# Optimization experiments

Measured on AMD Instinct MI355X. Metric: run time of the kernel, lower is better.

The kernel has to match this reference:

```python
import jax, jax.numpy as jnp
import numpy as np

N_NODES, N_EDGES, N_GRAPHS = 100000, 1600000, 1000
DIN, DMID, DGLOB, DOUT = 128, 128, 64, 2


def setup_inputs() -> dict:
    key = jax.random.key(0)
    ks = jax.random.split(key, 12)
    x = jax.random.normal(ks[0], (N_NODES, DIN), dtype=jnp.float32)
    edge_index = jax.random.randint(ks[1], (2, N_EDGES), 0, N_NODES, dtype=jnp.int64 if jax.config.jax_enable_x64 else jnp.int32)
    u = jax.random.normal(ks[2], (N_GRAPHS, DGLOB), dtype=jnp.float32)
    batch = jnp.sort(jax.random.randint(ks[3], (N_NODES,), 0, N_GRAPHS))
    s = 1.0 / np.sqrt(DMID)
    W1 = jax.random.normal(ks[4], (DIN, DMID), dtype=jnp.float32) * s
    b1 = jnp.zeros((DMID,), dtype=jnp.float32)
    W2 = jax.random.normal(ks[5], (DMID, DMID), dtype=jnp.float32) * s
    b2 = jnp.zeros((DMID,), dtype=jnp.float32)
    Wh1 = jax.random.normal(ks[6], (DMID + DGLOB, DMID), dtype=jnp.float32) * s
    bh1 = jnp.zeros((DMID,), dtype=jnp.float32)
    Wh2 = jax.random.normal(ks[7], (DMID, DOUT), dtype=jnp.float32) * s
    bh2 = jnp.zeros((DOUT,), dtype=jnp.float32)
    return {"x": x, "edge_index": edge_index, "u": u, "batch": batch,
            "batch_size": N_GRAPHS, "W1": W1, "b1": b1, "W2": W2, "b2": b2,
            "Wh1": Wh1, "bh1": bh1, "Wh2": Wh2, "bh2": bh2}


def _gcn_conv(x, W, b, row, col, norm, n):
    # PyG GCNConv: linear transform then symmetric-normalized scatter-add
    h = x @ W                                    # [N, dmid]
    msg = norm[:, None] * h[row]                 # gather along source nodes
    out = jax.ops.segment_sum(msg, col, num_segments=n)  # scatter to dst
    return out + b


def reference(x, edge_index, u, batch, batch_size, W1, b1, W2, b2, Wh1, bh1, Wh2, bh2):
    n = x.shape[0]
    # add self-loops (GCNConv default, edge_weight=None -> all-ones weights)
    loop = jnp.arange(n, dtype=edge_index.dtype)
    row = jnp.concatenate([edge_index[0], loop])
    col = jnp.concatenate([edge_index[1], loop])
    deg = jax.ops.segment_sum(jnp.ones_like(col, dtype=x.dtype), col, num_segments=n)
    dinv = jnp.where(deg > 0, jax.lax.rsqrt(jnp.maximum(deg, 1e-12)), 0.0)
    norm = dinv[row] * dinv[col]                 # D^-1/2 A D^-1/2, shared by both layers

    h = jax.nn.relu(_gcn_conv(x, W1, b1, row, col, norm, n))
    h = jax.nn.relu(_gcn_conv(h, W2, b2, row, col, norm, n))

    # mean pool per graph
    sums = jax.ops.segment_sum(h, batch, num_segments=batch_size)
    cnt = jax.ops.segment_sum(jnp.ones((n,), dtype=h.dtype), batch, num_segments=batch_size)
    graph_emb = sums / jnp.maximum(cnt, 1.0)[:, None]

    hcat = jnp.concatenate([graph_emb, u], axis=-1)
    # head MLP (dropout in eval mode = identity)
    out = jax.nn.relu(hcat @ Wh1 + bh1) @ Wh2 + bh2
    return out
```

## Files before the change

kernel.cpp:

```cpp
#include <hip/hip_runtime.h>
#include <hip/hip_bf16.h>

#define NN 100000
#define NE 1600000
#define NG 1000
#define NBK 196
#define BSH 9
#define SLOT 10240

typedef short short8 __attribute__((ext_vector_type(8)));
typedef float f32x4 __attribute__((ext_vector_type(4)));
typedef float f32x2 __attribute__((ext_vector_type(2)));

static inline int cdiv(int a, int b) { return (a + b - 1) / b; }

__device__ __forceinline__ unsigned short f2b(float f) {
    unsigned int u = __float_as_uint(f);
    u += 0x7fff + ((u >> 16) & 1);
    return (unsigned short)(u >> 16);
}
__device__ __forceinline__ unsigned int pack2(float lo, float hi) {
    return (unsigned int)f2b(lo) | ((unsigned int)f2b(hi) << 16);
}

template <int W>
__device__ __forceinline__ f32x2 f8_2f(unsigned int v) {
    return __builtin_amdgcn_cvt_pk_f32_fp8((int)v, W);
}
__device__ __forceinline__ unsigned int f2f8_lo(float a, float b, unsigned int old) {
    return (unsigned int)__builtin_amdgcn_cvt_pk_fp8_f32(a, b, (int)old, false);
}
__device__ __forceinline__ unsigned int f2f8_hi(float a, float b, unsigned int old) {
    return (unsigned int)__builtin_amdgcn_cvt_pk_fp8_f32(a, b, (int)old, true);
}
__device__ __forceinline__ unsigned char f2f8s(float a) {
    return (unsigned char)(__builtin_amdgcn_cvt_pk_fp8_f32(a, a, 0, false) & 0xFF);
}

__global__ __launch_bounds__(256) void k_prep(const float* __restrict__ W1,
                                              const float* __restrict__ W2,
                                              const float* __restrict__ b1,
                                              const float* __restrict__ b2,
                                              unsigned short* __restrict__ Wt1,
                                              unsigned char* __restrict__ Wt2p,
                                              float* __restrict__ b1p,
                                              float* __restrict__ b2p,
                                              int* __restrict__ gcur) {
    int b = blockIdx.x, t = threadIdx.x;
    if (b < 128) {
        if (t < 128) {
            Wt1[b * 128 + t] = f2b(W1[t * 128 + b]);
        } else {
            int q = t - 128;
            int c = (q & 7) * 16 + (q >> 3);
            Wt2p[b * 128 + q] = f2f8s(W2[c * 128 + b]);
        }
    } else {
        if (t < NBK) gcur[t] = t * SLOT;
        if (t < 128) {
            int c = (t & 7) * 16 + (t >> 3);
            b1p[t] = b1[c];
            b2p[t] = b2[c];
        }
    }
}

__global__ __launch_bounds__(256) void k_bin2(const int* __restrict__ row,
                                              const int* __restrict__ col,
                                              int* __restrict__ gcur,
                                              unsigned int* __restrict__ tmp) {
    __shared__ unsigned int ent[4000];
    __shared__ unsigned int srt[4000];
    __shared__ unsigned char bkt[4000];
    __shared__ unsigned char bky[4000];
    __shared__ int cnt[NBK];
    __shared__ int gbase[NBK];
    __shared__ int lbase[NBK];
    __shared__ int sh[256];
    int t = threadIdx.x;
    if (t < NBK) cnt[t] = 0;
    __syncthreads();
    const int q0 = blockIdx.x * 1000;
    const int4* col4 = (const int4*)col;
    const int4* row4 = (const int4*)row;
#pragma unroll
    for (int it = 0; it < 4; it++) {
        int idx = it * 256 + t;
        if (idx < 1000) {
            int4 c = col4[q0 + idx];
            int4 r = row4[q0 + idx];
            int d, b;
            d = c.x; b = d >> BSH; atomicAdd(&cnt[b], 1);
            ent[idx * 4 + 0] = ((unsigned int)(d & 511) << 17) | (unsigned int)r.x;
            bkt[idx * 4 + 0] = (unsigned char)b;
            d = c.y; b = d >> BSH; atomicAdd(&cnt[b], 1);
            ent[idx * 4 + 1] = ((unsigned int)(d & 511) << 17) | (unsigned int)r.y;
            bkt[idx * 4 + 1] = (unsigned char)b;
            d = c.z; b = d >> BSH; atomicAdd(&cnt[b], 1);
            ent[idx * 4 + 2] = ((unsigned int)(d & 511) << 17) | (unsigned int)r.z;
            bkt[idx * 4 + 2] = (unsigned char)b;
            d = c.w; b = d >> BSH; atomicAdd(&cnt[b], 1);
            ent[idx * 4 + 3] = ((unsigned int)(d & 511) << 17) | (unsigned int)r.w;
            bkt[idx * 4 + 3] = (unsigned char)b;
        }
    }
    __syncthreads();
    int v = (t < NBK) ? cnt[t] : 0;
    sh[t] = v;
    __syncthreads();
    for (int d = 1; d < 256; d <<= 1) {
        int u = (t >= d) ? sh[t - d] : 0;
        __syncthreads();
        sh[t] += u;
        __syncthreads();
    }
    if (t < NBK) {
        lbase[t] = sh[t] - v;
        gbase[t] = atomicAdd(&gcur[t], v);
        cnt[t] = sh[t] - v;
    }
    __syncthreads();
#pragma unroll
    for (int it = 0; it < 16; it++) {
        int i = it * 256 + t;
        if (i < 4000) {
            int b = bkt[i];
            int p = atomicAdd(&cnt[b], 1);
            srt[p] = ent[i];
            bky[p] = (unsigned char)b;
        }
    }
    __syncthreads();
#pragma unroll
    for (int it = 0; it < 16; it++) {
        int i = it * 256 + t;
        if (i < 4000) {
            int b = bky[i];
            tmp[gbase[b] + (i - lbase[b])] = srt[i];
        }
    }
}

__global__ __launch_bounds__(1024) void k_bucket(const unsigned int* __restrict__ tmp,
                                                 const int* __restrict__ gcur,
                                                 int* __restrict__ off,
                                                 int* __restrict__ degw,
                                                 float* __restrict__ dinv,
                                                 int* __restrict__ csr_src) {
    __shared__ int cnt[512];
    __shared__ int loff[512];
    __shared__ int sh[256];
    int b = blockIdx.x, t = threadIdx.x;
    int j0 = b << BSH;
    int nd = min(512, NN - j0);
    int rb = b * SLOT;
    int m = gcur[b] - rb;
    if (t < 512) cnt[t] = 0;
    __syncthreads();
    for (int i = t; i < m; i += 1024)
        atomicAdd(&cnt[tmp[rb + i] >> 17], 1);
    __syncthreads();
    int r0 = 0, r1 = 0, p0 = 0, ts = 0;
    if (t < 256) {
        r0 = cnt[2 * t]; r1 = cnt[2 * t + 1];
        p0 = (r0 + 3) & ~3;
        int p1 = (r1 + 3) & ~3;
        ts = p0 + p1;
        sh[t] = ts;
    }
    __syncthreads();
    for (int d = 1; d < 256; d <<= 1) {
        int u = (t >= d && t < 256) ? sh[t - d] : 0;
        __syncthreads();
        if (t < 256) sh[t] += u;
        __syncthreads();
    }
    if (t < 256) {
        int ex = sh[t] - ts;
        loff[2 * t] = ex;
        loff[2 * t + 1] = ex + p0;
    }
    __syncthreads();
    for (int j = t; j < nd; j += 1024) {
        int o = rb + loff[j];
        int dg = cnt[j];
        off[j0 + j] = o;
        degw[j0 + j] = dg;
        dinv[j0 + j] = rsqrtf((float)(dg + 1));
        cnt[j] = o;
    }
    __syncthreads();
    for (int i = t; i < m; i += 1024) {
        unsigned int e = tmp[rb + i];
        int d = e >> 17;
        int s = (int)(e & 0x1FFFFu);
        int p = atomicAdd(&cnt[d], 1);
        csr_src[p] = s;
    }
}

__global__ __launch_bounds__(256) void k_gemm1(const float* __restrict__ X,
                                               const unsigned short* __restrict__ Wt,
                                               const float* __restrict__ dinv,
                                               unsigned char* __restrict__ Hs8) {
    __shared__ __align__(16) unsigned short Ws[128 * 128];
    int t = threadIdx.x;
#pragma unroll
    for (int i = 0; i < 8; i++) {
        int id = t + i * 256;
        int n = id >> 4, c = id & 15;
        *(short8*)((char*)Ws + n * 256 + ((c ^ (n & 15)) << 4)) =
            *(const short8*)(Wt + n * 128 + c * 8);
    }
    __syncthreads();

    int lane = t & 63, wid = t >> 6;
    int n16 = lane & 15, quad = lane >> 4;
    int row_base = blockIdx.x * 128 + wid * 32;

    short8 a[2][4];
#pragma unroll
    for (int rt = 0; rt < 2; rt++) {
        int r = row_base + rt * 16 + n16;
        if (r > NN - 1) r = NN - 1;
        const float* ap = X + (size_t)r * 128 + quad * 8;
#pragma unroll
        for (int ks = 0; ks < 4; ks++) {
            float4 v0 = *(const float4*)(ap + ks * 32);
            float4 v1 = *(const float4*)(ap + ks * 32 + 4);
            uint4 up;
            up.x = pack2(v0.x, v0.y); up.y = pack2(v0.z, v0.w);
            up.z = pack2(v1.x, v1.y); up.w = pack2(v1.z, v1.w);
            a[rt][ks] = *(short8*)&up;
        }
    }

    f32x4 acc[2][8];
#pragma unroll
    for (int rt = 0; rt < 2; rt++)
#pragma unroll
        for (int ct = 0; ct < 8; ct++)
            acc[rt][ct] = (f32x4){0.f, 0.f, 0.f, 0.f};

#pragma unroll
    for (int ks = 0; ks < 4; ks++) {
#pragma unroll
        for (int ct = 0; ct < 8; ct++) {
            short8 b = *(const short8*)((const char*)Ws +
                        (ct * 16 + n16) * 256 + ((((ks << 2) + quad) ^ n16) << 4));
            acc[0][ct] = __builtin_amdgcn_mfma_f32_16x16x32_bf16(a[0][ks], b, acc[0][ct], 0, 0, 0);
            acc[1][ct] = __builtin_amdgcn_mfma_f32_16x16x32_bf16(a[1][ks], b, acc[1][ct], 0, 0, 0);
        }
    }

#pragma unroll
    for (int rt = 0; rt < 2; rt++) {
#pragma unroll
        for (int reg = 0; reg < 4; reg++) {
            int row = row_base + rt * 16 + quad * 4 + reg;
            if (row < NN) {
                float di = dinv[row];
                unsigned int u0 = 0, u1 = 0;
                u0 = f2f8_lo(acc[rt][0][reg] * di, acc[rt][1][reg] * di, u0);
                u0 = f2f8_hi(acc[rt][2][reg] * di, acc[rt][3][reg] * di, u0);
                u1 = f2f8_lo(acc[rt][4][reg] * di, acc[rt][5][reg] * di, u1);
                u1 = f2f8_hi(acc[rt][6][reg] * di, acc[rt][7][reg] * di, u1);
                uint2 o; o.x = u0; o.y = u1;
                ((uint2*)(Hs8 + (size_t)row * 128))[n16] = o;
            }
        }
    }
}

__global__ __launch_bounds__(256) void k_gemm2(const unsigned char* __restrict__ A8,
                                               const unsigned char* __restrict__ Wt2p,
                                               const float* __restrict__ dinv,
                                               unsigned char* __restrict__ Hs8) {
    __shared__ __align__(16) unsigned char Ws[128 * 128];
    int t = threadIdx.x;
#pragma unroll
    for (int i = 0; i < 8; i++) {
        int id = t + i * 256;
        int n = id >> 4, c = id & 15;
        *(uint2*)(Ws + n * 128 + ((c ^ (n & 15)) << 3)) =
            *(const uint2*)(Wt2p + n * 128 + c * 8);
    }
    __syncthreads();

    int lane = t & 63, wid = t >> 6;
    int n16 = lane & 15, quad = lane >> 4;
    int row_base = blockIdx.x * 128 + wid * 32;

    uint2 a[2][4];
#pragma unroll
    for (int rt = 0; rt < 2; rt++) {
        int r = row_base + rt * 16 + n16;
        if (r > NN - 1) r = NN - 1;
        const unsigned char* ap = A8 + (size_t)r * 128 + quad * 8;
#pragma unroll
        for (int ks = 0; ks < 4; ks++)
            a[rt][ks] = *(const uint2*)(ap + ks * 32);
    }

    f32x4 acc[2][8];
#pragma unroll
    for (int rt = 0; rt < 2; rt++)
#pragma unroll
        for (int ct = 0; ct < 8; ct++)
            acc[rt][ct] = (f32x4){0.f, 0.f, 0.f, 0.f};

#pragma unroll
    for (int ks = 0; ks < 4; ks++) {
        long a0 = __builtin_bit_cast(long, a[0][ks]);
        long a1 = __builtin_bit_cast(long, a[1][ks]);
#pragma unroll
        for (int ct = 0; ct < 8; ct++) {
            uint2 bv = *(const uint2*)(Ws + (ct * 16 + n16) * 128 +
                                       ((((ks << 2) + quad) ^ n16) << 3));
            long bb = __builtin_bit_cast(long, bv);
            acc[0][ct] = __builtin_amdgcn_mfma_f32_16x16x32_fp8_fp8(a0, bb, acc[0][ct], 0, 0, 0);
            acc[1][ct] = __builtin_amdgcn_mfma_f32_16x16x32_fp8_fp8(a1, bb, acc[1][ct], 0, 0, 0);
        }
    }

#pragma unroll
    for (int rt = 0; rt < 2; rt++) {
#pragma unroll
        for (int reg = 0; reg < 4; reg++) {
            int row = row_base + rt * 16 + quad * 4 + reg;
            if (row < NN) {
                float di = dinv[row];
                unsigned int u0 = 0, u1 = 0;
                u0 = f2f8_lo(acc[rt][0][reg] * di, acc[rt][1][reg] * di, u0);
                u0 = f2f8_hi(acc[rt][2][reg] * di, acc[rt][3][reg] * di, u0);
                u1 = f2f8_lo(acc[rt][4][reg] * di, acc[rt][5][reg] * di, u1);
                u1 = f2f8_hi(acc[rt][6][reg] * di, acc[rt][7][reg] * di, u1);
                uint2 o; o.x = u0; o.y = u1;
                ((uint2*)(Hs8 + (size_t)row * 128))[n16] = o;
            }
        }
    }
}

__global__ __launch_bounds__(256) void k_agg(const unsigned char* __restrict__ Hb,
                                             const int* __restrict__ off,
                                             const int* __restrict__ degw,
                                             const int* __restrict__ csr_src,
                                             const float* __restrict__ dinv,
                                             const float* __restrict__ biasp,
                                             unsigned char* __restrict__ outp) {
    int node = blockIdx.x * 4 + (threadIdx.x >> 6);
    int lane = threadIdx.x & 63;
    int sub = lane >> 4, li = lane & 15;
    unsigned loff = (unsigned)li * 8u;
    f32x2 A0 = {0.f, 0.f}, A1 = {0.f, 0.f}, A2 = {0.f, 0.f}, A3 = {0.f, 0.f};
#define LDH(idx) (*(const uint2*)(Hb + (unsigned)(idx) * 128u + loff))
#define ACC8(V) { \
        A0 += f8_2f<0>((V).x); A1 += f8_2f<1>((V).x); \
        A2 += f8_2f<0>((V).y); A3 += f8_2f<1>((V).y); }
    int deg = degw[node];
    int base = off[node];
    int slot = sub * 4;
    int4 iA = *(const int4*)(csr_src + base + slot);
    int4 iB;
    bool hasB = deg > 16;
    if (hasB) iB = *(const int4*)(csr_src + base + 16 + slot);
    uint2 v = {0, 0};
    if (sub == 0) v = LDH(node);
    uint2 w0 = {0,0}, w1 = {0,0}, w2 = {0,0}, w3 = {0,0};
    uint2 w4 = {0,0}, w5 = {0,0}, w6 = {0,0}, w7 = {0,0};
    if (slot + 0 < deg) w0 = LDH(iA.x);
    if (slot + 1 < deg) w1 = LDH(iA.y);
    if (slot + 2 < deg) w2 = LDH(iA.z);
    if (slot + 3 < deg) w3 = LDH(iA.w);
    if (hasB) {
        if (slot + 16 < deg) w4 = LDH(iB.x);
        if (slot + 17 < deg) w5 = LDH(iB.y);
        if (slot + 18 < deg) w6 = LDH(iB.z);
        if (slot + 19 < deg) w7 = LDH(iB.w);
    }
    ACC8(v)
    ACC8(w0) ACC8(w1) ACC8(w2) ACC8(w3)
    if (hasB) { ACC8(w4) ACC8(w5) ACC8(w6) ACC8(w7) }
    if (deg > 32) {
        int e = base + 32, e1 = base + deg;
        for (; e + 16 <= e1; e += 16) {
            int4 sv = *(const int4*)(csr_src + e + sub * 4);
            uint2 x0 = LDH(sv.x);
            uint2 x1 = LDH(sv.y);
            uint2 x2 = LDH(sv.z);
            uint2 x3 = LDH(sv.w);
            ACC8(x0) ACC8(x1) ACC8(x2) ACC8(x3)
        }
        for (; e + 8 <= e1; e += 8) {
            int2 sv = *(const int2*)(csr_src + e + sub * 2);
            uint2 xA = LDH(sv.x);
            uint2 xB = LDH(sv.y);
            ACC8(xA) ACC8(xB)
        }
        for (; e < e1; e += 4) {
            int ee = e + sub;
            if (ee < e1) {
                uint2 w = LDH(csr_src[ee]);
                ACC8(w)
            }
        }
    }
#undef ACC8
#undef LDH
#pragma unroll
    for (int d = 16; d <= 32; d <<= 1) {
        A0[0] += __shfl_xor(A0[0], d); A0[1] += __shfl_xor(A0[1], d);
        A1[0] += __shfl_xor(A1[0], d); A1[1] += __shfl_xor(A1[1], d);
        A2[0] += __shfl_xor(A2[0], d); A2[1] += __shfl_xor(A2[1], d);
        A3[0] += __shfl_xor(A3[0], d); A3[1] += __shfl_xor(A3[1], d);
    }
    if (sub == 0) {
        float di = dinv[node];
        const float4* b4 = (const float4*)biasp;
        float4 bA = b4[li * 2], bB = b4[li * 2 + 1];
        float r0 = fmaxf(fmaf(di, A0[0], bA.x), 0.f);
        float r1 = fmaxf(fmaf(di, A0[1], bA.y), 0.f);
        float r2 = fmaxf(fmaf(di, A1[0], bA.z), 0.f);
        float r3 = fmaxf(fmaf(di, A1[1], bA.w), 0.f);
        float r4 = fmaxf(fmaf(di, A2[0], bB.x), 0.f);
        float r5 = fmaxf(fmaf(di, A2[1], bB.y), 0.f);
        float r6 = fmaxf(fmaf(di, A3[0], bB.z), 0.f);
        float r7 = fmaxf(fmaf(di, A3[1], bB.w), 0.f);
        unsigned int u0 = 0, u1 = 0;
        u0 = f2f8_lo(r0, r1, u0); u0 = f2f8_hi(r2, r3, u0);
        u1 = f2f8_lo(r4, r5, u1); u1 = f2f8_hi(r6, r7, u1);
        uint2 o; o.x = u0; o.y = u1;
        *(uint2*)(outp + (unsigned)node * 128u + loff) = o;
    }
}

__global__ __launch_bounds__(256) void k_poolhead(const unsigned char* __restrict__ A,
                                                  const int* __restrict__ batch,
                                                  const float* __restrict__ u,
                                                  const float* __restrict__ Wh1,
                                                  const float* __restrict__ bh1,
                                                  const float* __restrict__ Wh2,
                                                  const float* __restrict__ bh2,
                                                  float* __restrict__ out) {
    int g = blockIdx.x, t = threadIdx.x;
    int lo = 0, hi = NN;
    while (lo < hi) { int m = (lo + hi) >> 1; if (batch[m] < g) lo = m + 1; else hi = m; }
    int start = lo;
    hi = NN;
    while (lo < hi) { int m = (lo + hi) >> 1; if (batch[m] < g + 1) lo = m + 1; else hi = m; }
    int end = lo;

    int li = t & 7;
    int ri = t >> 3;
    float acc[16];
#pragma unroll
    for (int j = 0; j < 16; j++) acc[j] = 0.f;
    f32x2 p;
    for (int i = start + ri; i < end; i += 32) {
        uint4 v = ((const uint4*)A)[(size_t)i * 8 + li];
#define UP(VV, base) p = f8_2f<0>(VV); acc[base] += p.x; acc[base+1] += p.y; \
                     p = f8_2f<1>(VV); acc[base+2] += p.x; acc[base+3] += p.y;
        UP(v.x, 0) UP(v.y, 4) UP(v.z, 8) UP(v.w, 12)
#undef UP
    }
#pragma unroll
    for (int j = 0; j < 16; j++) {
        acc[j] += __shfl_xor(acc[j], 8);
        acc[j] += __shfl_xor(acc[j], 16);
        acc[j] += __shfl_xor(acc[j], 32);
    }
    __shared__ float part[4][128];
    __shared__ float hc[192];
    __shared__ float tt[128];
    int w = t >> 6;
    if ((t & 63) < 8) {
#pragma unroll
        for (int j = 0; j < 16; j++) part[w][li * 16 + j] = acc[j];
    }
    __syncthreads();
    float cntf = (float)max(end - start, 1);
    if (t < 128) {
        int q = (t & 15) * 8 + (t >> 4);
        hc[t] = (part[0][q] + part[1][q] + part[2][q] + part[3][q]) / cntf;
    } else if (t < 192) {
        hc[t] = u[g * 64 + (t - 128)];
    }
    __syncthreads();
    if (t < 128) {
        float a2 = bh1[t];
        for (int k = 0; k < 192; k++) a2 = fmaf(hc[k], Wh1[k * 128 + t], a2);
        tt[t] = fmaxf(a2, 0.f);
    }
    __syncthreads();
    if (t < 2) {
        float o = bh2[t];
        for (int c2 = 0; c2 < 128; c2++) o = fmaf(tt[c2], Wh2[c2 * 2 + t], o);
        out[g * 2 + t] = o;
    }
}

extern "C" void kernel_launch(void* const* d_in, const int* in_sizes, int n_in,
                              void* d_out, int out_size, void* d_ws, size_t ws_size,
                              hipStream_t stream) {
    const float* x   = (const float*)d_in[0];
    const int*   ei  = (const int*)d_in[1];
    const int*   row = ei;
    const int*   col = ei + NE;
    const float* u   = (const float*)d_in[2];
    const int*   batch = (const int*)d_in[3];
    const float* W1  = (const float*)d_in[5];
    const float* b1  = (const float*)d_in[6];
    const float* W2  = (const float*)d_in[7];
    const float* b2  = (const float*)d_in[8];
    const float* Wh1 = (const float*)d_in[9];
    const float* bh1 = (const float*)d_in[10];
    const float* Wh2 = (const float*)d_in[11];
    const float* bh2 = (const float*)d_in[12];
    float* out = (float*)d_out;

    char* ws = (char*)d_ws;
    size_t o = 0;
    auto alloc = [&](size_t bytes) -> void* {
        void* p = ws + o;
        o += (bytes + 511) & ~(size_t)511;
        return p;
    };
    unsigned char*  Hs8 = (unsigned char*)alloc((size_t)NN * 128);
    unsigned char*  A1b = (unsigned char*)alloc((size_t)NN * 128);
    unsigned char*  A2b = (unsigned char*)alloc((size_t)NN * 128);
    unsigned short* Wt1 = (unsigned short*)alloc((size_t)128 * 128 * 2);
    unsigned char*  Wt2p= (unsigned char*)alloc((size_t)128 * 128);
    float* b1p    = (float*)alloc((size_t)128 * 4);
    float* b2p    = (float*)alloc((size_t)128 * 4);
    float* dinv   = (float*)alloc((size_t)NN * 4);
    int*   off    = (int*)alloc((size_t)NN * 4);
    int*   degw   = (int*)alloc((size_t)NN * 4);
    int*   csr_src= (int*)alloc((size_t)NBK * SLOT * 4 + 256);
    unsigned int* tmp = (unsigned int*)alloc((size_t)NBK * SLOT * 4);
    int*   gcur   = (int*)alloc((size_t)256 * 4);

    k_prep<<<129, 256, 0, stream>>>(W1, W2, b1, b2, Wt1, Wt2p, b1p, b2p, gcur);
    k_bin2<<<400, 256, 0, stream>>>(row, col, gcur, tmp);
    k_bucket<<<NBK, 1024, 0, stream>>>(tmp, gcur, off, degw, dinv, csr_src);

    k_gemm1<<<cdiv(NN, 128), 256, 0, stream>>>(x, Wt1, dinv, Hs8);
    k_agg<<<NN / 4, 256, 0, stream>>>(Hs8, off, degw, csr_src, dinv, b1p, A1b);
    k_gemm2<<<cdiv(NN, 128), 256, 0, stream>>>(A1b, Wt2p, dinv, Hs8);
    k_agg<<<NN / 4, 256, 0, stream>>>(Hs8, off, degw, csr_src, dinv, b2p, A2b);

    k_poolhead<<<NG, 256, 0, stream>>>(A2b, batch, u, Wh1, bh1, Wh2, bh2, out);
}
```

Before: 267.6 us.

## Use 16-lane group per node in aggregation; precompute graph start offsets

The aggregation kernel now assigns one 16-lane group to each node (16 nodes per block) instead of a full 64-lane wavefront that split edges four ways and reduced them with cross-lane shuffles. Each group walks its node's edges sequentially in chunks of four, which removes the shuffle reduction and the idle lanes during the epilogue. The trade-off is less memory-level parallelism per node and longer serial loops for high-degree nodes. Separately, k_prep gains extra blocks that compute per-graph start offsets from the sorted batch array, so the pooling kernel no longer runs two binary searches per graph.

Measured after the change: 259.3 us. 3.1% less time.

```diff
diff --git a/kernel.cpp b/kernel.cpp
--- a/kernel.cpp
+++ b/kernel.cpp
@@ -45,7 +45,9 @@
                                               unsigned char* __restrict__ Wt2p,
                                               float* __restrict__ b1p,
                                               float* __restrict__ b2p,
-                                              int* __restrict__ gcur) {
+                                              int* __restrict__ gcur,
+                                              const int* __restrict__ batch,
+                                              int* __restrict__ gstart) {
     int b = blockIdx.x, t = threadIdx.x;
     if (b < 128) {
         if (t < 128) {
@@ -55,12 +57,19 @@
             int c = (q & 7) * 16 + (q >> 3);
             Wt2p[b * 128 + q] = f2f8s(W2[c * 128 + b]);
         }
-    } else {
+    } else if (b == 128) {
         if (t < NBK) gcur[t] = t * SLOT;
         if (t < 128) {
             int c = (t & 7) * 16 + (t >> 3);
             b1p[t] = b1[c];
             b2p[t] = b2[c];
+        }
+    } else {
+        int n = (b - 129) * 256 + t;
+        if (n <= NN) {
+            int cur = (n == NN) ? NG : batch[n];
+            int prev = (n == 0) ? -1 : batch[n - 1];
+            for (int g = prev + 1; g <= cur; g++) gstart[g] = n;
         }
     }
 }
@@ -349,9 +358,8 @@
                                              const float* __restrict__ dinv,
                                              const float* __restrict__ biasp,
                                              unsigned char* __restrict__ outp) {
-    int node = blockIdx.x * 4 + (threadIdx.x >> 6);
-    int lane = threadIdx.x & 63;
-    int sub = lane >> 4, li = lane & 15;
+    int node = blockIdx.x * 16 + (threadIdx.x >> 4);
+    int li = threadIdx.x & 15;
     unsigned loff = (unsigned)li * 8u;
     f32x2 A0 = {0.f, 0.f}, A1 = {0.f, 0.f}, A2 = {0.f, 0.f}, A3 = {0.f, 0.f};
 #define LDH(idx) (*(const uint2*)(Hb + (unsigned)(idx) * 128u + loff))
@@ -360,83 +368,39 @@
         A2 += f8_2f<0>((V).y); A3 += f8_2f<1>((V).y); }
     int deg = degw[node];
     int base = off[node];
-    int slot = sub * 4;
-    int4 iA = *(const int4*)(csr_src + base + slot);
-    int4 iB;
-    bool hasB = deg > 16;
-    if (hasB) iB = *(const int4*)(csr_src + base + 16 + slot);
-    uint2 v = {0, 0};
-    if (sub == 0) v = LDH(node);
-    uint2 w0 = {0,0}, w1 = {0,0}, w2 = {0,0}, w3 = {0,0};
-    uint2 w4 = {0,0}, w5 = {0,0}, w6 = {0,0}, w7 = {0,0};
-    if (slot + 0 < deg) w0 = LDH(iA.x);
-    if (slot + 1 < deg) w1 = LDH(iA.y);
-    if (slot + 2 < deg) w2 = LDH(iA.z);
-    if (slot + 3 < deg) w3 = LDH(iA.w);
-    if (hasB) {
-        if (slot + 16 < deg) w4 = LDH(iB.x);
-        if (slot + 17 < deg) w5 = LDH(iB.y);
-        if (slot + 18 < deg) w6 = LDH(iB.z);
-        if (slot + 19 < deg) w7 = LDH(iB.w);
-    }
+    uint2 v = LDH(node);
     ACC8(v)
-    ACC8(w0) ACC8(w1) ACC8(w2) ACC8(w3)
-    if (hasB) { ACC8(w4) ACC8(w5) ACC8(w6) ACC8(w7) }
-    if (deg > 32) {
-        int e = base + 32, e1 = base + deg;
-        for (; e + 16 <= e1; e += 16) {
-            int4 sv = *(const int4*)(csr_src + e + sub * 4);
-            uint2 x0 = LDH(sv.x);
-            uint2 x1 = LDH(sv.y);
-            uint2 x2 = LDH(sv.z);
-            uint2 x3 = LDH(sv.w);
-            ACC8(x0) ACC8(x1) ACC8(x2) ACC8(x3)
-        }
-        for (; e + 8 <= e1; e += 8) {
-            int2 sv = *(const int2*)(csr_src + e + sub * 2);
-            uint2 xA = LDH(sv.x);
-            uint2 xB = LDH(sv.y);
-            ACC8(xA) ACC8(xB)
-        }
-        for (; e < e1; e += 4) {
-            int ee = e + sub;
-            if (ee < e1) {
-                uint2 w = LDH(csr_src[ee]);
-                ACC8(w)
-            }
-        }
+    for (int e = 0; e < deg; e += 4) {
+        int4 ix = *(const int4*)(csr_src + base + e);
+        uint2 w0 = LDH(ix.x);
+        uint2 w1 = {0, 0}, w2 = {0, 0}, w3 = {0, 0};
+        if (e + 1 < deg) w1 = LDH(ix.y);
+        if (e + 2 < deg) w2 = LDH(ix.z);
+        if (e + 3 < deg) w3 = LDH(ix.w);
+        ACC8(w0) ACC8(w1) ACC8(w2) ACC8(w3)
     }
 #undef ACC8
 #undef LDH
-#pragma unroll
-    for (int d = 16; d <= 32; d <<= 1) {
-        A0[0] += __shfl_xor(A0[0], d); A0[1] += __shfl_xor(A0[1], d);
-        A1[0] += __shfl_xor(A1[0], d); A1[1] += __shfl_xor(A1[1], d);
-        A2[0] += __shfl_xor(A2[0], d); A2[1] += __shfl_xor(A2[1], d);
-        A3[0] += __shfl_xor(A3[0], d); A3[1] += __shfl_xor(A3[1], d);
-    }
-    if (sub == 0) {
-        float di = dinv[node];
-        const float4* b4 = (const float4*)biasp;
-        float4 bA = b4[li * 2], bB = b4[li * 2 + 1];
-        float r0 = fmaxf(fmaf(di, A0[0], bA.x), 0.f);
-        float r1 = fmaxf(fmaf(di, A0[1], bA.y), 0.f);
-        float r2 = fmaxf(fmaf(di, A1[0], bA.z), 0.f);
-        float r3 = fmaxf(fmaf(di, A1[1], bA.w), 0.f);
-        float r4 = fmaxf(fmaf(di, A2[0], bB.x), 0.f);
-        float r5 = fmaxf(fmaf(di, A2[1], bB.y), 0.f);
-        float r6 = fmaxf(fmaf(di, A3[0], bB.z), 0.f);
-        float r7 = fmaxf(fmaf(di, A3[1], bB.w), 0.f);
-        unsigned int u0 = 0, u1 = 0;
-        u0 = f2f8_lo(r0, r1, u0); u0 = f2f8_hi(r2, r3, u0);
-        u1 = f2f8_lo(r4, r5, u1); u1 = f2f8_hi(r6, r7, u1);
-        uint2 o; o.x = u0; o.y = u1;
-        *(uint2*)(outp + (unsigned)node * 128u + loff) = o;
-    }
+    float di = dinv[node];
+    const float4* b4 = (const float4*)biasp;
+    float4 bA = b4[li * 2], bB = b4[li * 2 + 1];
+    float r0 = fmaxf(fmaf(di, A0[0], bA.x), 0.f);
+    float r1 = fmaxf(fmaf(di, A0[1], bA.y), 0.f);
+    float r2 = fmaxf(fmaf(di, A1[0], bA.z), 0.f);
+    float r3 = fmaxf(fmaf(di, A1[1], bA.w), 0.f);
+    float r4 = fmaxf(fmaf(di, A2[0], bB.x), 0.f);
+    float r5 = fmaxf(fmaf(di, A2[1], bB.y), 0.f);
+    float r6 = fmaxf(fmaf(di, A3[0], bB.z), 0.f);
+    float r7 = fmaxf(fmaf(di, A3[1], bB.w), 0.f);
+    unsigned int u0 = 0, u1 = 0;
+    u0 = f2f8_lo(r0, r1, u0); u0 = f2f8_hi(r2, r3, u0);
+    u1 = f2f8_lo(r4, r5, u1); u1 = f2f8_hi(r6, r7, u1);
+    uint2 o; o.x = u0; o.y = u1;
+    *(uint2*)(outp + (unsigned)node * 128u + loff) = o;
 }
 
 __global__ __launch_bounds__(256) void k_poolhead(const unsigned char* __restrict__ A,
-                                                  const int* __restrict__ batch,
+                                                  const int* __restrict__ gstart,
                                                   const float* __restrict__ u,
                                                   const float* __restrict__ Wh1,
                                                   const float* __restrict__ bh1,
@@ -444,12 +408,8 @@
                                                   const float* __restrict__ bh2,
                                                   float* __restrict__ out) {
     int g = blockIdx.x, t = threadIdx.x;
-    int lo = 0, hi = NN;
-    while (lo < hi) { int m = (lo + hi) >> 1; if (batch[m] < g) lo = m + 1; else hi = m; }
-    int start = lo;
-    hi = NN;
-    while (lo < hi) { int m = (lo + hi) >> 1; if (batch[m] < g + 1) lo = m + 1; else hi = m; }
-    int end = lo;
+    int start = gstart[g];
+    int end = gstart[g + 1];
 
     int li = t & 7;
     int ri = t >> 3;
@@ -539,15 +499,17 @@
     int*   csr_src= (int*)alloc((size_t)NBK * SLOT * 4 + 256);
     unsigned int* tmp = (unsigned int*)alloc((size_t)NBK * SLOT * 4);
     int*   gcur   = (int*)alloc((size_t)256 * 4);
-
-    k_prep<<<129, 256, 0, stream>>>(W1, W2, b1, b2, Wt1, Wt2p, b1p, b2p, gcur);
+    int*   gstart = (int*)alloc((size_t)(NG + 1) * 4);
+
+    k_prep<<<129 + cdiv(NN + 1, 256), 256, 0, stream>>>(W1, W2, b1, b2, Wt1, Wt2p,
+                                                        b1p, b2p, gcur, batch, gstart);
     k_bin2<<<400, 256, 0, stream>>>(row, col, gcur, tmp);
     k_bucket<<<NBK, 1024, 0, stream>>>(tmp, gcur, off, degw, dinv, csr_src);
 
     k_gemm1<<<cdiv(NN, 128), 256, 0, stream>>>(x, Wt1, dinv, Hs8);
-    k_agg<<<NN / 4, 256, 0, stream>>>(Hs8, off, degw, csr_src, dinv, b1p, A1b);
+    k_agg<<<NN / 16, 256, 0, stream>>>(Hs8, off, degw, csr_src, dinv, b1p, A1b);
     k_gemm2<<<cdiv(NN, 128), 256, 0, stream>>>(A1b, Wt2p, dinv, Hs8);
-    k_agg<<<NN / 4, 256, 0, stream>>>(Hs8, off, degw, csr_src, dinv, b2p, A2b);
-
-    k_poolhead<<<NG, 256, 0, stream>>>(A2b, batch, u, Wh1, bh1, Wh2, bh2, out);
-}
+    k_agg<<<NN / 16, 256, 0, stream>>>(Hs8, off, degw, csr_src, dinv, b2p, A2b);
+
+    k_poolhead<<<NG, 256, 0, stream>>>(A2b, gstart, u, Wh1, bh1, Wh2, bh2, out);
+}
```
